# Optimization experiments

Measured on AMD Instinct MI355X. Metric: run time of the kernel, lower is better.

The kernel has to match this reference:

```python
import jax, jax.numpy as jnp
import numpy as np

B, N, DIM, H, DH = 2, 2048, 1024, 16, 64
ALPHA = 32.0 ** 2  # stable_softmax alpha
SCALE = DH ** -0.5


def rotate_half(x):
    # interleaved pairs: (x0, x1, x2, x3, ...) -> (-x1, x0, -x3, x2, ...)
    xp = x.reshape(x.shape[:-1] + (-1, 2))
    return jnp.stack((-xp[..., 1], xp[..., 0]), axis=-1).reshape(x.shape)


def apply_rotary(freqs, t):
    # freqs: [n, d]; t: [b, h, n, d]
    return t * jnp.cos(freqs) + rotate_half(t) * jnp.sin(freqs)


def setup_inputs() -> dict:
    key = jax.random.key(0)
    k0, k1, k2, k3 = jax.random.split(key, 4)
    x = jax.random.normal(k0, (B, N, DIM), jnp.float32)
    rotary_pos_emb = jax.random.normal(k1, (N, DH), jnp.float32)
    w_qkv = jax.random.normal(k2, (DIM, 3 * H * DH), jnp.float32) / np.sqrt(DIM)
    w_out = jax.random.normal(k3, (H * DH, DIM), jnp.float32) / np.sqrt(H * DH)
    b_out = jnp.zeros((DIM,), jnp.float32)
    return {"x": x, "rotary_pos_emb": rotary_pos_emb, "w_qkv": w_qkv,
            "w_out": w_out, "b_out": b_out}


def reference(x, rotary_pos_emb, w_qkv, w_out, b_out):
    b, n, _ = x.shape
    qkv = x @ w_qkv                                  # [b, n, 3*h*d]
    q, k, v = jnp.split(qkv, 3, axis=-1)
    to_heads = lambda t: t.reshape(b, n, H, DH).transpose(0, 2, 1, 3)  # [b,h,n,d]
    q, k, v = map(to_heads, (q, k, v))
    freqs = rotary_pos_emb[:n]
    # source applies rotary emb to q, k AND v
    q = apply_rotary(freqs, q)
    k = apply_rotary(freqs, k)
    v = apply_rotary(freqs, v)
    q = q * SCALE
    dots = jnp.einsum('bhid,bhjd->bhij', q, k)       # [b,h,n,n]
    mask_value = -jnp.finfo(dots.dtype).max
    causal = jnp.triu(jnp.ones((n, n), bool), 1)
    dots = jnp.where(causal, mask_value, dots)
    # stable softmax: divide by alpha, subtract detached max, rescale
    t = dots / ALPHA
    t = t - jax.lax.stop_gradient(jnp.max(t, axis=-1, keepdims=True))
    attn = jax.nn.softmax(t * ALPHA, axis=-1)
    out = jnp.einsum('bhij,bhjd->bhid', attn, v)     # [b,h,n,d]
    out = out.transpose(0, 2, 1, 3).reshape(b, n, H * DH)
    return out @ w_out + b_out
```

## Files before the change

### kernel.cpp

```cpp
#include <hip/hip_runtime.h>
#include <stdint.h>

#define DEV __device__ __forceinline__

typedef __bf16 bf16x8 __attribute__((ext_vector_type(8)));
typedef float  f32x4  __attribute__((ext_vector_type(4)));
typedef short  s16x8  __attribute__((ext_vector_type(8)));

constexpr int Bb   = 2;
constexpr int Nn   = 2048;
constexpr int DIMc = 1024;
constexpr int Hh   = 16;
constexpr int DHc  = 64;
constexpr int BN   = Bb * Nn;
constexpr int QKVC = 3 * Hh * DHc;

DEV ushort f2b(float f) {
  uint32_t u = __float_as_uint(f);
  u += 0x7fffu + ((u >> 16) & 1u);
  return (ushort)(u >> 16);
}

DEV void gload16(const void* g, void* l) {
  __builtin_amdgcn_global_load_lds(
      (const __attribute__((address_space(1))) void*)(uintptr_t)g,
      (__attribute__((address_space(3))) void*)(uint32_t)(uintptr_t)l,
      16, 0, 0);
}

DEV f32x4 mfma16(bf16x8 a, bf16x8 b, f32x4 c) {
  return __builtin_amdgcn_mfma_f32_16x16x32_bf16(a, b, c, 0, 0, 0);
}

DEV uint32_t cvtpk(float lo, float hi) {
  uint32_t r;
  asm("v_cvt_pk_bf16_f32 %0, %1, %2" : "=v"(r) : "v"(lo), "v"(hi));
  return r;
}


__global__ void k_cast_x(const float* __restrict__ x, ushort* __restrict__ xb,
                         const float* __restrict__ rope, float2* __restrict__ csT) {
  int i = blockIdx.x * 256 + threadIdx.x;
  size_t base = (size_t)i * 8;
  s16x8 v;
#pragma unroll
  for (int j = 0; j < 8; ++j) v[j] = (short)f2b(x[base + j]);
  *(s16x8*)(xb + base) = v;
  if (i < Nn * DHc) {
    float t = rope[i];
    float s, c;
    sincosf(t, &s, &c);
    csT[i] = make_float2(c, s);
  }
}

__global__ void k_transpose_cast(const float* __restrict__ src, ushort* __restrict__ dst,
                                 int K, int Ncols) {
  __shared__ float tile[32][33];
  int nb = blockIdx.x * 32, kb = blockIdx.y * 32;
  int tx = threadIdx.x, ty = threadIdx.y;
#pragma unroll
  for (int i = 0; i < 4; ++i) {
    int k = ty + i * 8;
    tile[k][tx] = src[(size_t)(kb + k) * Ncols + nb + tx];
  }
  __syncthreads();
#pragma unroll
  for (int i = 0; i < 4; ++i) {
    int n = ty + i * 8;
    dst[(size_t)(nb + n) * K + kb + tx] = f2b(tile[tx][n]);
  }
}

DEV void gemm_core(const ushort* __restrict__ A, const ushort* __restrict__ Bt,
                   int rowBase, int colBase, ushort* lA, ushort* lB,
                   f32x4 (&acc)[4][4]) {
  const int tid = threadIdx.x;
  const int lane = tid & 63, w = tid >> 6;
  const int wm = w >> 1, wn = w & 1;
  const int g = lane >> 4, l16 = lane & 15;
  const f32x4 zero = {0.f, 0.f, 0.f, 0.f};
#pragma unroll
  for (int i = 0; i < 4; ++i)
#pragma unroll
    for (int j = 0; j < 4; ++j) acc[i][j] = zero;

  const int c0row = tid >> 2,          c0kc = (tid & 3) ^ ((c0row >> 1) & 3);
  const int c1row = (256 + tid) >> 2,  c1kc = (tid & 3) ^ ((c1row >> 1) & 3);
  const ushort* gA0 = A  + (size_t)(rowBase + c0row) * DIMc + c0kc * 8;
  const ushort* gA1 = A  + (size_t)(rowBase + c1row) * DIMc + c1kc * 8;
  const ushort* gB0 = Bt + (size_t)(colBase + c0row) * DIMc + c0kc * 8;
  const ushort* gB1 = Bt + (size_t)(colBase + c1row) * DIMc + c1kc * 8;
  const size_t o0 = (size_t)(0 * 256 + w * 64) * 8;
  const size_t o1 = (size_t)(1 * 256 + w * 64) * 8;
  constexpr int BUF = 128 * 32;

  gload16(gA0,      lA + o0);        gload16(gB0,      lB + o0);
  gload16(gA1,      lA + o1);        gload16(gB1,      lB + o1);
  gload16(gA0 + 32, lA + BUF + o0);  gload16(gB0 + 32, lB + BUF + o0);
  gload16(gA1 + 32, lA + BUF + o1);  gload16(gB1 + 32, lB + BUF + o1);
  asm volatile("s_waitcnt vmcnt(4)" ::: "memory");
  __builtin_amdgcn_s_barrier();

  int cur = 0;
  for (int k0 = 0; k0 < DIMc; k0 += 32) {
    const ushort* cA = lA + cur * BUF;
    const ushort* cB = lB + cur * BUF;

    bf16x8 af[4], bfr[4];
#pragma unroll
    for (int f = 0; f < 4; ++f) {
      int r  = wm * 64 + f * 16 + l16;
      int r2 = wn * 64 + f * 16 + l16;
      af[f]  = *(const bf16x8*)&cA[r  * 32 + ((g ^ ((r  >> 1) & 3)) << 3)];
      bfr[f] = *(const bf16x8*)&cB[r2 * 32 + ((g ^ ((r2 >> 1) & 3)) << 3)];
    }

    const int kn = k0 + 64;
    if (kn < DIMc) {
      int st = cur + 2; if (st >= 3) st -= 3;
      ushort* nA = lA + st * BUF;
      ushort* nB = lB + st * BUF;
      gload16(gA0 + kn, nA + o0);  gload16(gB0 + kn, nB + o0);
      gload16(gA1 + kn, nA + o1);  gload16(gB1 + kn, nB + o1);
    }

#pragma unroll
    for (int i = 0; i < 4; ++i)
#pragma unroll
      for (int j = 0; j < 4; ++j)
        acc[i][j] = mfma16(af[i], bfr[j], acc[i][j]);

    if (kn < DIMc) {
      asm volatile("s_waitcnt vmcnt(4)" ::: "memory");
    } else if (k0 + 32 < DIMc) {
      asm volatile("s_waitcnt vmcnt(0)" ::: "memory");
    }
    asm volatile("s_waitcnt lgkmcnt(0)" ::: "memory");
    __builtin_amdgcn_s_barrier();
    cur += 1; if (cur == 3) cur = 0;
  }
}

__global__ __launch_bounds__(256) void k_gemm_qkv(
    const ushort* __restrict__ xb, const ushort* __restrict__ wT,
    const float2* __restrict__ csT,
    ushort* __restrict__ Qd, ushort* __restrict__ Kd, ushort* __restrict__ Vd) {
  __shared__ ushort lA[3 * 128 * 32];
  __shared__ ushort lB[3 * 128 * 32];
  f32x4 acc[4][4];
  const int rowBase = blockIdx.y * 128, colBase = blockIdx.x * 128;
  gemm_core(xb, wT, rowBase, colBase, lA, lB, acc);

  const int lane = threadIdx.x & 63, w = threadIdx.x >> 6;
  const int wm = w >> 1, wn = w & 1;
  const int g = lane >> 4, l16 = lane & 15;
#pragma unroll
  for (int fm = 0; fm < 4; ++fm) {
#pragma unroll
    for (int fn = 0; fn < 4; ++fn) {
      int col = colBase + wn * 64 + fn * 16 + l16;
      int sel = col >> 10, hc = col & 1023;
      int h = hc >> 6, d = hc & 63;
      float sgn = (d & 1) ? 1.f : -1.f;
#pragma unroll
      for (int r = 0; r < 4; ++r) {
        float t  = acc[fm][fn][r];
        float tp = __shfl_xor(t, 1);
        int row = rowBase + wm * 64 + fm * 16 + 4 * g + r;
        int b = row >> 11, n = row & 2047;
        float2 cs = csT[n * 64 + d];
        float rv = t * cs.x + sgn * tp * cs.y;
        if (sel == 0) {
          Qd[((size_t)(b * Hh + h) * Nn + n) * DHc + d] = f2b(rv * 0.125f);
        } else if (sel == 1) {
          Kd[((size_t)(b * Hh + h) * Nn + n) * DHc + d] = f2b(rv);
        } else {
          Vd[((size_t)(b * Hh + h) * DHc + d) * Nn + n] = f2b(rv);
        }
      }
    }
  }
}


DEV void stageKV(const ushort* __restrict__ Kh, const ushort* __restrict__ Vh,
                 ushort* lKb, ushort* lVb, int kt, int tid, int w) {
#pragma unroll
  for (int s = 0; s < 2; ++s) {
    int c = s * 256 + tid;
    int row = c >> 3, jst = c & 7;
    int jl = jst ^ (row & 7);
    gload16(Kh + (size_t)(kt * 64 + row) * DHc + jl * 8,
            lKb + (size_t)(s * 256 + w * 64) * 8);
    gload16(Vh + (size_t)row * Nn + kt * 64 + jl * 8,
            lVb + (size_t)(s * 256 + w * 64) * 8);
  }
}

DEV void attn_step(const ushort* lKc, const ushort* lVc, char* lPw,
                   const bf16x8 (&q)[2], f32x4 (&o)[4], float& m, float& l,
                   int kBase, int qg, bool diag, int g, int l16) {
  const f32x4 zero = {0.f, 0.f, 0.f, 0.f};
  f32x4 s[4];
#pragma unroll
  for (int jt = 0; jt < 4; ++jt) s[jt] = zero;

#pragma unroll
  for (int jt = 0; jt < 4; ++jt) {
    int jr = jt * 16 + l16;
#pragma unroll
    for (int d0 = 0; d0 < 2; ++d0) {
      bf16x8 kb = *(const bf16x8*)&lKc[jr * 64 + (((d0 * 4 + g) ^ (jr & 7)) << 3)];
      s[jt] = mfma16(kb, q[d0], s[jt]);
    }
  }

  if (diag) {
#pragma unroll
    for (int jt = 0; jt < 4; ++jt)
#pragma unroll
      for (int r = 0; r < 4; ++r) {
        int j = kBase + jt * 16 + 4 * g + r;
        if (j > qg) s[jt][r] = -3.0e38f;
      }
  }

  float tmax = fmaxf(fmaxf(fmaxf(s[0][0], s[0][1]), fmaxf(s[0][2], s[0][3])),
                     fmaxf(fmaxf(s[1][0], s[1][1]), fmaxf(s[1][2], s[1][3])));
  tmax = fmaxf(tmax, fmaxf(fmaxf(fmaxf(s[2][0], s[2][1]), fmaxf(s[2][2], s[2][3])),
                           fmaxf(fmaxf(s[3][0], s[3][1]), fmaxf(s[3][2], s[3][3]))));
  tmax = fmaxf(tmax, __shfl_xor(tmax, 16));
  tmax = fmaxf(tmax, __shfl_xor(tmax, 32));

  if (!__all(tmax <= m + 8.f)) {
    float mnew = fmaxf(m, tmax);
    float sc = __expf(m - mnew);
#pragma unroll
    for (int dt = 0; dt < 4; ++dt) o[dt] *= sc;
    l *= sc;
    m = mnew;
  }

  float ps = 0.f;
#pragma unroll
  for (int jt = 0; jt < 4; ++jt)
#pragma unroll
    for (int r = 0; r < 4; ++r) {
      float p = __expf(s[jt][r] - m);
      s[jt][r] = p;
      ps += p;
    }
  ps += __shfl_xor(ps, 16);
  ps += __shfl_xor(ps, 32);
  l += ps;

  const int sw = (l16 & 7) << 4;
  char* prow = lPw + l16 * 128;
#pragma unroll
  for (int jt = 0; jt < 4; ++jt) {
    int jo = (jt * 16 + 4 * g) * 2;
    *(uint32_t*)(prow + (jo ^ sw))       = cvtpk(s[jt][0], s[jt][1]);
    *(uint32_t*)(prow + ((jo + 4) ^ sw)) = cvtpk(s[jt][2], s[jt][3]);
  }

  bf16x8 pa[2];
#pragma unroll
  for (int jh = 0; jh < 2; ++jh)
    pa[jh] = *(const bf16x8*)(prow + (((jh * 32 + 8 * g) * 2) ^ sw));
#pragma unroll
  for (int dt = 0; dt < 4; ++dt) {
    int d = dt * 16 + l16;
#pragma unroll
    for (int jh = 0; jh < 2; ++jh) {
      bf16x8 vb = *(const bf16x8*)&lVc[d * 64 + (((jh * 4 + g) ^ (d & 7)) << 3)];
      o[dt] = mfma16(vb, pa[jh], o[dt]);
    }
  }
}

DEV void attn_epi(ushort* __restrict__ ao, int bh, int n, int g,
                  f32x4 (&o)[4], float l) {
  const int b = bh >> 4, h = bh & 15;
  float inv = 1.f / l;
  ushort* dst = ao + (size_t)(b * Nn + n) * (Hh * DHc) + h * 64;
#pragma unroll
  for (int dt = 0; dt < 4; ++dt) {
    uint2 pkd;
    pkd.x = cvtpk(o[dt][0] * inv, o[dt][1] * inv);
    pkd.y = cvtpk(o[dt][2] * inv, o[dt][3] * inv);
    *(uint2*)(dst + dt * 16 + 4 * g) = pkd;
  }
}

__global__ __launch_bounds__(256) void k_attn(
    const ushort* __restrict__ Qd, const ushort* __restrict__ Kd,
    const ushort* __restrict__ Vd, ushort* __restrict__ ao) {
  __shared__ ushort lK[2][64 * 64];
  __shared__ ushort lV[2][64 * 64];
  __shared__ char   lP[4][16 * 128];
  const int tid = threadIdx.x;
  const int lane = tid & 63, w = tid >> 6;
  const int g = lane >> 4, l16 = lane & 15;
  const int bh = blockIdx.y;
  const int qt = 31 - blockIdx.x;
  const int last = qt;
  const ushort* Qh = Qd + (size_t)bh * Nn * DHc;
  const ushort* Kh = Kd + (size_t)bh * Nn * DHc;
  const ushort* Vh = Vd + (size_t)bh * DHc * Nn;

  const int qg = qt * 64 + w * 16 + l16;

  bf16x8 q[2];
#pragma unroll
  for (int d0 = 0; d0 < 2; ++d0)
    q[d0] = *(const bf16x8*)(Qh + (size_t)qg * DHc + d0 * 32 + g * 8);

  const f32x4 zero = {0.f, 0.f, 0.f, 0.f};
  f32x4 o[4];
#pragma unroll
  for (int dt = 0; dt < 4; ++dt) o[dt] = zero;
  float m = -3.0e38f, l = 0.f;

  stageKV(Kh, Vh, lK[0], lV[0], 0, tid, w);

  for (int kt = 0; kt <= last; ++kt) {
    const int cur = kt & 1;
    if (kt < last) {
      stageKV(Kh, Vh, lK[cur ^ 1], lV[cur ^ 1], kt + 1, tid, w);
      asm volatile("s_waitcnt vmcnt(4)" ::: "memory");
    } else {
      asm volatile("s_waitcnt vmcnt(0)" ::: "memory");
    }
    __builtin_amdgcn_s_barrier();

    attn_step(lK[cur], lV[cur], lP[w], q, o, m, l, kt * 64, qg, kt == last, g, l16);

    __builtin_amdgcn_s_barrier();
  }

  attn_epi(ao, bh, qg, g, o, l);
}

__global__ __launch_bounds__(256) void k_gemm_out(
    const ushort* __restrict__ ao, const ushort* __restrict__ wT,
    const float* __restrict__ bias, float* __restrict__ out) {
  __shared__ ushort lA[3 * 64 * 32];
  __shared__ ushort lB[3 * 128 * 32];
  const int tid = threadIdx.x;
  const int lane = tid & 63, w = tid >> 6;
  const int g = lane >> 4, l16 = lane & 15;
  const int rowBase = blockIdx.y * 64, colBase = blockIdx.x * 128;

  f32x4 acc[4][2];
  const f32x4 zero = {0.f, 0.f, 0.f, 0.f};
#pragma unroll
  for (int i = 0; i < 4; ++i) { acc[i][0] = zero; acc[i][1] = zero; }

  const int arow = tid >> 2, akc = (tid & 3) ^ ((arow >> 1) & 3);
  const int b1row = 64 + arow, b1kc = (tid & 3) ^ ((b1row >> 1) & 3);
  const ushort* gA  = ao + (size_t)(rowBase + arow) * DIMc + akc * 8;
  const ushort* gB0 = wT + (size_t)(colBase + arow) * DIMc + akc * 8;
  const ushort* gB1 = wT + (size_t)(colBase + b1row) * DIMc + b1kc * 8;
  const size_t oA  = (size_t)w * 512;
  const size_t oB0 = (size_t)w * 512;
  const size_t oB1 = 2048 + (size_t)w * 512;
  constexpr int BUFA = 64 * 32, BUFB = 128 * 32;

  gload16(gA,      lA + oA);         gload16(gB0,      lB + oB0);         gload16(gB1,      lB + oB1);
  gload16(gA + 32, lA + BUFA + oA);  gload16(gB0 + 32, lB + BUFB + oB0);  gload16(gB1 + 32, lB + BUFB + oB1);
  asm volatile("s_waitcnt vmcnt(3)" ::: "memory");
  __builtin_amdgcn_s_barrier();

  int cur = 0;
  for (int k0 = 0; k0 < DIMc; k0 += 32) {
    const ushort* cA = lA + cur * BUFA;
    const ushort* cB = lB + cur * BUFB;

    bf16x8 af[4], bfr[2];
#pragma unroll
    for (int f = 0; f < 4; ++f) {
      int r = f * 16 + l16;
      af[f] = *(const bf16x8*)&cA[r * 32 + ((g ^ ((r >> 1) & 3)) << 3)];
    }
#pragma unroll
    for (int f = 0; f < 2; ++f) {
      int r2 = w * 32 + f * 16 + l16;
      bfr[f] = *(const bf16x8*)&cB[r2 * 32 + ((g ^ ((r2 >> 1) & 3)) << 3)];
    }

    const int kn = k0 + 64;
    if (kn < DIMc) {
      int st = cur + 2; if (st >= 3) st -= 3;
      gload16(gA + kn,  lA + st * BUFA + oA);
      gload16(gB0 + kn, lB + st * BUFB + oB0);
      gload16(gB1 + kn, lB + st * BUFB + oB1);
    }

#pragma unroll
    for (int i = 0; i < 4; ++i)
#pragma unroll
      for (int j = 0; j < 2; ++j)
        acc[i][j] = mfma16(af[i], bfr[j], acc[i][j]);

    if (kn < DIMc) {
      asm volatile("s_waitcnt vmcnt(3)" ::: "memory");
    } else if (k0 + 32 < DIMc) {
      asm volatile("s_waitcnt vmcnt(0)" ::: "memory");
    }
    asm volatile("s_waitcnt lgkmcnt(0)" ::: "memory");
    __builtin_amdgcn_s_barrier();
    cur += 1; if (cur == 3) cur = 0;
  }

#pragma unroll
  for (int fm = 0; fm < 4; ++fm)
#pragma unroll
    for (int fn = 0; fn < 2; ++fn) {
      int col = colBase + w * 32 + fn * 16 + l16;
#pragma unroll
      for (int r = 0; r < 4; ++r) {
        int row = rowBase + fm * 16 + 4 * g + r;
        out[(size_t)row * DIMc + col] = acc[fm][fn][r] + bias[col];
      }
    }
}

extern "C" void kernel_launch(void* const* d_in, const int* in_sizes, int n_in,
                              void* d_out, int out_size, void* d_ws, size_t ws_size,
                              hipStream_t stream) {
  const float* x     = (const float*)d_in[0];
  const float* rope  = (const float*)d_in[1];
  const float* w_qkv = (const float*)d_in[2];
  const float* w_out = (const float*)d_in[3];
  const float* b_out = (const float*)d_in[4];
  float* out = (float*)d_out;

  char* ws = (char*)d_ws;
  ushort* xb    = (ushort*)(ws);
  ushort* wqkvT = (ushort*)(ws + 8388608);
  ushort* woutT = (ushort*)(ws + 14680064);
  float2* csT   = (float2*)(ws + 16777216);
  ushort* Qd    = (ushort*)(ws + 17825792);
  ushort* Kd    = (ushort*)(ws + 26214400);
  ushort* Vd    = (ushort*)(ws + 34603008);
  ushort* ao    = (ushort*)(ws + 42991616);

  hipLaunchKernelGGL(k_cast_x, dim3(2048), dim3(256), 0, stream, x, xb, rope, csT);
  hipLaunchKernelGGL(k_transpose_cast, dim3(QKVC / 32, DIMc / 32), dim3(32, 8), 0, stream,
                     w_qkv, wqkvT, DIMc, QKVC);
  hipLaunchKernelGGL(k_transpose_cast, dim3(DIMc / 32, DIMc / 32), dim3(32, 8), 0, stream,
                     w_out, woutT, DIMc, DIMc);
  hipLaunchKernelGGL(k_gemm_qkv, dim3(QKVC / 128, BN / 128), dim3(256), 0, stream,
                     xb, wqkvT, csT, Qd, Kd, Vd);
  hipLaunchKernelGGL(k_attn, dim3(32, Bb * Hh), dim3(256), 0, stream, Qd, Kd, Vd, ao);
  hipLaunchKernelGGL(k_gemm_out, dim3(DIMc / 128, BN / 64), dim3(256), 0, stream,
                     ao, woutT, b_out, out);
}
```

Baseline: 149.4 us.

## Split attention KV loop across two wave groups with flash-decoding style merge

The attention kernel grows to 512 threads, forming two groups of four waves that share the same query tile. The groups process alternating KV tiles (even and odd) out of a double-buffered pair of LDS slots, which halves the serial KV loop per block. At the end, the partial (o, m, l) states are merged through LDS using a log-sum-exp rescale. This adds LDS usage, extra merge work and a barrier, and lowers occupancy per CU in exchange for more parallelism on the long causal rows.

```diff
diff --git a/kernel.cpp b/kernel.cpp
--- a/kernel.cpp
+++ b/kernel.cpp
@@ -185,18 +185,18 @@
 }
 
 
-DEV void stageKV(const ushort* __restrict__ Kh, const ushort* __restrict__ Vh,
-                 ushort* lKb, ushort* lVb, int kt, int tid, int w) {
-#pragma unroll
-  for (int s = 0; s < 2; ++s) {
-    int c = s * 256 + tid;
-    int row = c >> 3, jst = c & 7;
-    int jl = jst ^ (row & 7);
-    gload16(Kh + (size_t)(kt * 64 + row) * DHc + jl * 8,
-            lKb + (size_t)(s * 256 + w * 64) * 8);
-    gload16(Vh + (size_t)row * Nn + kt * 64 + jl * 8,
-            lVb + (size_t)(s * 256 + w * 64) * 8);
-  }
+DEV void stageKVpair(const ushort* __restrict__ Kh, const ushort* __restrict__ Vh,
+                     ushort* lK0, ushort* lK1, ushort* lV0, ushort* lV1,
+                     int pj, int qt, int tid, int w) {
+  int row = tid >> 3, jst = tid & 7;
+  int jl = jst ^ (row & 7);
+  int t0 = 2 * pj;     if (t0 > qt) t0 = qt;
+  int t1 = 2 * pj + 1; if (t1 > qt) t1 = qt;
+  const size_t lo = (size_t)(w * 64) * 8;
+  gload16(Kh + (size_t)(t0 * 64 + row) * DHc + jl * 8, lK0 + lo);
+  gload16(Kh + (size_t)(t1 * 64 + row) * DHc + jl * 8, lK1 + lo);
+  gload16(Vh + (size_t)row * Nn + t0 * 64 + jl * 8,    lV0 + lo);
+  gload16(Vh + (size_t)row * Nn + t1 * 64 + jl * 8,    lV1 + lo);
 }
 
 DEV void attn_step(const ushort* lKc, const ushort* lVc, char* lPw,
@@ -294,23 +294,24 @@
   }
 }
 
-__global__ __launch_bounds__(256) void k_attn(
+__global__ __launch_bounds__(512) void k_attn(
     const ushort* __restrict__ Qd, const ushort* __restrict__ Kd,
     const ushort* __restrict__ Vd, ushort* __restrict__ ao) {
-  __shared__ ushort lK[2][64 * 64];
-  __shared__ ushort lV[2][64 * 64];
-  __shared__ char   lP[4][16 * 128];
+  __shared__ ushort lK[2][2][64 * 64];
+  __shared__ ushort lV[2][2][64 * 64];
+  __shared__ char   lP[8][16 * 128];
   const int tid = threadIdx.x;
   const int lane = tid & 63, w = tid >> 6;
+  const int grp = w >> 2, ws = w & 3;
   const int g = lane >> 4, l16 = lane & 15;
   const int bh = blockIdx.y;
   const int qt = 31 - blockIdx.x;
-  const int last = qt;
+  const int npairs = (qt + 2) >> 1;
   const ushort* Qh = Qd + (size_t)bh * Nn * DHc;
   const ushort* Kh = Kd + (size_t)bh * Nn * DHc;
   const ushort* Vh = Vd + (size_t)bh * DHc * Nn;
 
-  const int qg = qt * 64 + w * 16 + l16;
+  const int qg = qt * 64 + ws * 16 + l16;
 
   bf16x8 q[2];
 #pragma unroll
@@ -323,24 +324,48 @@
   for (int dt = 0; dt < 4; ++dt) o[dt] = zero;
   float m = -3.0e38f, l = 0.f;
 
-  stageKV(Kh, Vh, lK[0], lV[0], 0, tid, w);
-
-  for (int kt = 0; kt <= last; ++kt) {
-    const int cur = kt & 1;
-    if (kt < last) {
-      stageKV(Kh, Vh, lK[cur ^ 1], lV[cur ^ 1], kt + 1, tid, w);
+  stageKVpair(Kh, Vh, lK[0][0], lK[0][1], lV[0][0], lV[0][1], 0, qt, tid, w);
+
+  for (int pj = 0; pj < npairs; ++pj) {
+    const int cur = pj & 1;
+    if (pj + 1 < npairs) {
+      stageKVpair(Kh, Vh, lK[cur ^ 1][0], lK[cur ^ 1][1], lV[cur ^ 1][0], lV[cur ^ 1][1],
+                  pj + 1, qt, tid, w);
       asm volatile("s_waitcnt vmcnt(4)" ::: "memory");
     } else {
       asm volatile("s_waitcnt vmcnt(0)" ::: "memory");
     }
     __builtin_amdgcn_s_barrier();
 
-    attn_step(lK[cur], lV[cur], lP[w], q, o, m, l, kt * 64, qg, kt == last, g, l16);
+    const int t = 2 * pj + grp;
+    if (t <= qt)
+      attn_step(lK[cur][grp], lV[cur][grp], lP[w], q, o, m, l, t * 64, qg, t == qt, g, l16);
 
     __builtin_amdgcn_s_barrier();
   }
 
-  attn_epi(ao, bh, qg, g, o, l);
+  float* mrg = (float*)&lK[0][0][0];
+  const int slot = (ws * 64 + lane) * 20;
+  if (grp == 1) {
+#pragma unroll
+    for (int dt = 0; dt < 4; ++dt)
+      *(f32x4*)(mrg + slot + dt * 4) = o[dt];
+    mrg[slot + 16] = m;
+    mrg[slot + 17] = l;
+  }
+  __builtin_amdgcn_s_barrier();
+  if (grp == 0) {
+    float m1 = mrg[slot + 16], l1 = mrg[slot + 17];
+    float mm = fmaxf(m, m1);
+    float a0 = __expf(m - mm), a1 = __expf(m1 - mm);
+    float ll = l * a0 + l1 * a1;
+#pragma unroll
+    for (int dt = 0; dt < 4; ++dt) {
+      f32x4 o1 = *(const f32x4*)(mrg + slot + dt * 4);
+      o[dt] = o[dt] * a0 + o1 * a1;
+    }
+    attn_epi(ao, bh, qg, g, o, ll);
+  }
 }
 
 __global__ __launch_bounds__(256) void k_gemm_out(
@@ -454,7 +479,7 @@
                      w_out, woutT, DIMc, DIMc);
   hipLaunchKernelGGL(k_gemm_qkv, dim3(QKVC / 128, BN / 128), dim3(256), 0, stream,
                      xb, wqkvT, csT, Qd, Kd, Vd);
-  hipLaunchKernelGGL(k_attn, dim3(32, Bb * Hh), dim3(256), 0, stream, Qd, Kd, Vd, ao);
+  hipLaunchKernelGGL(k_attn, dim3(32, Bb * Hh), dim3(512), 0, stream, Qd, Kd, Vd, ao);
   hipLaunchKernelGGL(k_gemm_out, dim3(DIMc / 128, BN / 64), dim3(256), 0, stream,
                      ao, woutT, b_out, out);
 }
```

Result: faster. 146.3 us (-2.1%).
